# Kernel optimization log

Measured on AMD Instinct MI355X. Metric: run time of the kernel, lower is better.

## Reference

```python
import jax, jax.numpy as jnp
import numpy as np

N = 40000      # nodes
E = 640000     # edges (avg degree 16)
IN = 128       # in_dim
H = 8          # n_heads
D = 16         # out_dim per head
ED = 64        # edge_dim
C = H * D      # out_channel = 128 == IN -> residual is Identity
EPS = 1e-5


def setup_inputs() -> dict:
    key = jax.random.key(0)
    ks = jax.random.split(key, 20)

    def lin(k, shape):
        fan_in = shape[-1]
        return jax.random.normal(k, shape, dtype=jnp.float32) / np.sqrt(fan_in)

    return {
        "q": jax.random.normal(ks[0], (N, IN), dtype=jnp.float32),
        "k": jax.random.normal(ks[1], (N, IN), dtype=jnp.float32),
        "v": jax.random.normal(ks[2], (N, IN), dtype=jnp.float32),
        "edge_feat": jax.random.normal(ks[3], (E, ED), dtype=jnp.float32),
        "src": jax.random.randint(ks[4], (E,), 0, N, dtype=jnp.int32),
        "dst": jax.random.randint(ks[5], (E,), 0, N, dtype=jnp.int32),
        "Wq": lin(ks[6], (C, IN)),
        "Wk": lin(ks[7], (C, IN)),
        "Wv": lin(ks[8], (C, IN)),
        "We": lin(ks[9], (H, ED)),
        "be": jnp.zeros((H,), dtype=jnp.float32),
        "Wo": lin(ks[10], (C, C)),
        "W1": lin(ks[11], (2 * C, C)),
        "b1": jnp.zeros((2 * C,), dtype=jnp.float32),
        "W2": lin(ks[12], (C, 2 * C)),
        "b2": jnp.zeros((C,), dtype=jnp.float32),
        "g1": jnp.ones((C,), dtype=jnp.float32),
        "bt1": jnp.zeros((C,), dtype=jnp.float32),
        "g2": jnp.ones((C,), dtype=jnp.float32),
        "bt2": jnp.zeros((C,), dtype=jnp.float32),
    }


def _batch_norm(x, g, b):
    mu = x.mean(axis=0)
    var = x.var(axis=0)  # biased, matching torch BN normalization
    return (x - mu) * jax.lax.rsqrt(var + EPS) * g + b


def reference(q, k, v, edge_feat, src, dst, Wq, Wk, Wv, We, be, Wo,
              W1, b1, W2, b2, g1, bt1, g2, bt2):
    n = q.shape[0]
    qd = (q @ Wq.T).reshape(n, H, D)        # [N,H,D] dst queries
    ksrc = (k @ Wk.T).reshape(-1, H, D)     # [N,H,D]
    vsrc = (v @ Wv.T).reshape(-1, H, D)     # [N,H,D]

    # per-edge attention scores: v_dot_u(q_dst, k_src) / sqrt(D)
    scores = jnp.einsum('ehd,ehd->eh', qd[dst], ksrc[src]) / jnp.sqrt(jnp.float32(D))
    # edge_mode == 'ADD': add per-head edge bias
    scores = scores + edge_feat @ We.T + be  # [E,H]

    # edge softmax normalized by destination node (segment softmax)
    smax = jax.ops.segment_max(scores, dst, num_segments=n)      # [N,H]
    ex = jnp.exp(scores - smax[dst])
    denom = jax.ops.segment_sum(ex, dst, num_segments=n)         # [N,H]
    attn = ex / denom[dst]                                       # [E,H]

    # scatter-weighted aggregation: sum_e attn * v_src -> dst
    agg = jax.ops.segment_sum(attn[:, :, None] * vsrc[src], dst, num_segments=n)  # [N,H,D]

    rst = agg.reshape(n, C) @ Wo.T
    rst = rst + q                    # residual (Identity: in_dim == out_channel)
    rst = _batch_norm(rst, g1, bt1)

    h = jnp.maximum(rst @ W1.T + b1, 0.0) @ W2.T + b2  # FFN
    rst = _batch_norm(h + rst, g2, bt2)
    return rst
```

## Files before the change

### kernel.cpp

```cpp
#include <hip/hip_runtime.h>
#include <cstdint>
#include <cstddef>

#define Nn 40000
#define Ne 640000
#define CC 128
#define EPSbn 1e-5f

typedef __attribute__((ext_vector_type(8))) __bf16 bf16x8;
typedef __attribute__((ext_vector_type(4))) float floatx4;

__device__ inline unsigned short f2bf(float x){
  union { float f; unsigned u; } c; c.f = x;
  unsigned r = c.u + 0x7fffu + ((c.u >> 16) & 1u);
  return (unsigned short)(r >> 16);
}
__device__ inline float bflo(unsigned u){ return __uint_as_float(u << 16); }
__device__ inline float bfhi(unsigned u){ return __uint_as_float(u & 0xffff0000u); }

__device__ inline unsigned f2e4m3(float x){
  unsigned u = __float_as_uint(x);
  unsigned s = (u >> 24) & 0x80u;
  unsigned a = u & 0x7fffffffu;
  unsigned lsb = (a >> 20) & 1u;
  a += 0x0007FFFFu + lsb;
  int e = (int)((a >> 23) & 0xffu) - 127;
  unsigned b;
  if (e < -9)      b = 0u;
  else if (e < -6) b = (unsigned)(int)rintf(__uint_as_float(u & 0x7fffffffu) * 512.f);
  else if (e > 8)  b = 0x7Eu;
  else             b = (unsigned)(((e + 7) << 3) | ((a >> 20) & 7u));
  if ((b & 0x7fu) == 0x7fu) b = 0x7Eu;
  return s | b;
}

#if defined(__has_builtin)
#if __has_builtin(__builtin_amdgcn_cvt_f32_fp8)
#define FP8_HW 1
#endif
#endif
template<int SEL>
__device__ inline float fp8dec(unsigned w){
#ifdef FP8_HW
  return __builtin_amdgcn_cvt_f32_fp8((int)w, SEL);
#else
  unsigned b = (w >> (SEL*8)) & 0xffu;
  unsigned s = (b & 0x80u) << 24;
  unsigned em = b & 0x7fu;
  float v;
  if (em >= 8) v = __uint_as_float((((em >> 3) + 117u) << 23)) * (float)(8 + (em & 7));
  else         v = (float)em * 0.001953125f;
  return __uint_as_float(__float_as_uint(v) | s);
#endif
}

__global__ void zero_k(int* __restrict__ p, int n){
  int i = blockIdx.x*blockDim.x + threadIdx.x;
  if (i < n) p[i] = 0;
}

struct GA3 {
  const void* A0; const void* A1; const void* A2;
  const float* W0; const float* W1; const float* W2;
  void* C0; void* C1; void* C2;
  int m0, m1, m2;
};

template<int KTILES,bool ABF16,bool HASBIAS,bool HASRES,bool RELU,bool AFFA,bool AFFRES,bool BNSTAT>
__global__ __launch_bounds__(256,2) void mgemm_k(
    GA3 ga, const float* __restrict__ bias, const float* __restrict__ res,
    const float* __restrict__ sc, const float* __restrict__ sh,
    float* __restrict__ bnS, float* __restrict__ bnQ,
    int M, int Ncols)
{
  constexpr int K = KTILES * 128;
  __shared__ __align__(16) unsigned short As[128*136];
  __shared__ __align__(16) unsigned short Ws[128*136];
  const int z = blockIdx.z;
  const void*  Ap = (z==0) ? ga.A0 : (z==1) ? ga.A1 : ga.A2;
  const float* W  = (z==0) ? ga.W0 : (z==1) ? ga.W1 : ga.W2;
  void*        Cp = (z==0) ? ga.C0 : (z==1) ? ga.C1 : ga.C2;
  const int mode  = (z==0) ? ga.m0 : (z==1) ? ga.m1 : ga.m2;

  const int tid  = threadIdx.x;
  const int lane = tid & 63;
  const int wv   = tid >> 6;
  const int m    = lane & 15;
  const int quad = lane >> 4;
  const int row0 = blockIdx.x * 128;
  const int col0 = blockIdx.y * 128;
  floatx4 acc[2][8] = {};

  for (int kt = 0; kt < K; kt += 128) {
    #pragma unroll 4
    for (int it = 0; it < 16; ++it) {
      int s = tid + it*256;
      int r = s >> 5;
      int c = (s & 31) << 2;
      int gr = row0 + r; if (gr >= M) gr = M - 1;
      ushort4 ua;
      if (ABF16) {
        ua = *(const ushort4*)((const unsigned short*)Ap + (size_t)gr*K + kt + c);
      } else {
        float4 a4 = *(const float4*)((const float*)Ap + (size_t)gr*K + kt + c);
        if (AFFA) {
          int kk = kt + c;
          a4.x = a4.x*sc[kk  ] + sh[kk  ];
          a4.y = a4.y*sc[kk+1] + sh[kk+1];
          a4.z = a4.z*sc[kk+2] + sh[kk+2];
          a4.w = a4.w*sc[kk+3] + sh[kk+3];
        }
        ua.x = f2bf(a4.x); ua.y = f2bf(a4.y); ua.z = f2bf(a4.z); ua.w = f2bf(a4.w);
      }
      *(ushort4*)&As[r*136 + c] = ua;
      float4 w4 = *(const float4*)(W + (size_t)(col0 + r)*K + kt + c);
      ushort4 uw;
      uw.x = f2bf(w4.x); uw.y = f2bf(w4.y); uw.z = f2bf(w4.z); uw.w = f2bf(w4.w);
      *(ushort4*)&Ws[r*136 + c] = uw;
    }
    __syncthreads();
    #pragma unroll
    for (int ks = 0; ks < 4; ++ks) {
      int ko = ks*32 + quad*8;
      bf16x8 a0 = *(const bf16x8*)&As[(32*wv      + m)*136 + ko];
      bf16x8 a1 = *(const bf16x8*)&As[(32*wv + 16 + m)*136 + ko];
      #pragma unroll
      for (int j = 0; j < 8; ++j) {
        bf16x8 bj = *(const bf16x8*)&Ws[(16*j + m)*136 + ko];
        acc[0][j] = __builtin_amdgcn_mfma_f32_16x16x32_bf16(a0, bj, acc[0][j], 0, 0, 0);
        acc[1][j] = __builtin_amdgcn_mfma_f32_16x16x32_bf16(a1, bj, acc[1][j], 0, 0, 0);
      }
    }
    __syncthreads();
  }

  float bcol[8], scv[8], shv[8];
  #pragma unroll
  for (int j = 0; j < 8; ++j) {
    int gcol = col0 + 16*j + m;
    if (HASBIAS) bcol[j] = bias[gcol];
    if (AFFRES) { scv[j] = sc[gcol]; shv[j] = sh[gcol]; }
  }
  float ps[8] = {}, pq[8] = {};
  #pragma unroll
  for (int rt = 0; rt < 2; ++rt) {
    #pragma unroll
    for (int rg = 0; rg < 4; ++rg) {
      int grow = row0 + 32*wv + 16*rt + quad*4 + rg;
      if (grow < M) {
        #pragma unroll
        for (int j = 0; j < 8; ++j) {
          int gcol = col0 + 16*j + m;
          float o = acc[rt][j][rg];
          if (HASBIAS) o += bcol[j];
          if (HASRES) {
            float rr = res[(size_t)grow*Ncols + gcol];
            if (AFFRES) rr = rr*scv[j] + shv[j];
            o += rr;
          }
          if (RELU) o = fmaxf(o, 0.f);
          if (BNSTAT) { ps[j] += o; pq[j] += o*o; }
          if (mode == 0) ((float*)Cp)[(size_t)grow*Ncols + gcol] = o;
          else           ((unsigned short*)Cp)[(size_t)grow*Ncols + gcol] = f2bf(o);
        }
      }
    }
  }
  if (BNSTAT) {
    float* sS = (float*)&As[0];
    float* sQ = sS + 4*128;
    #pragma unroll
    for (int j = 0; j < 8; ++j) {
      float s = ps[j], qq = pq[j];
      s += __shfl_xor(s, 16); qq += __shfl_xor(qq, 16);
      s += __shfl_xor(s, 32); qq += __shfl_xor(qq, 32);
      if (quad == 0) { sS[wv*128 + 16*j + m] = s; sQ[wv*128 + 16*j + m] = qq; }
    }
    __syncthreads();
    if (wv == 0) {
      #pragma unroll
      for (int c = 0; c < 128; c += 64) {
        int cc = c + lane;
        float s  = sS[cc] + sS[128+cc] + sS[256+cc] + sS[384+cc];
        float qq = sQ[cc] + sQ[128+cc] + sQ[256+cc] + sQ[384+cc];
        atomicAdd(&bnS[col0 + cc], s);
        atomicAdd(&bnQ[col0 + cc], qq);
      }
    }
  }
}

__global__ __launch_bounds__(256) void repack_k(
    const unsigned* __restrict__ Kb, const unsigned* __restrict__ Vb,
    unsigned* __restrict__ KV, int total)
{
  int i = blockIdx.x*blockDim.x + threadIdx.x;
  if (i < total) {
    unsigned kk = Kb[i];
    unsigned vv = Vb[i];
    unsigned o = f2e4m3(bflo(kk)) | (f2e4m3(bfhi(kk)) << 8)
               | (f2e4m3(bflo(vv)) << 16) | (f2e4m3(bfhi(vv)) << 24);
    KV[i] = o;
  }
}

__global__ __launch_bounds__(256) void ebias_k(
    const float* __restrict__ ef, const float* __restrict__ We,
    const float* __restrict__ be, const int* __restrict__ pos,
    unsigned short* __restrict__ EBs)
{
  __shared__ float efs[32][68];
  __shared__ float Wes[8][68];
  __shared__ float bes[8];
  int tid = threadIdx.x;
  if (tid < 8) bes[tid] = be[tid];
  for (int i = tid; i < 512; i += 256) Wes[i>>6][i&63] = We[i];
  int e0 = blockIdx.x * 32;
  #pragma unroll
  for (int l = 0; l < 2; ++l) {
    int idx = tid + l*256;
    int r   = idx >> 4;
    int q4  = (idx & 15) << 2;
    float4 t = *(const float4*)(ef + (size_t)(e0 + r)*64 + q4);
    efs[r][q4]=t.x; efs[r][q4+1]=t.y; efs[r][q4+2]=t.z; efs[r][q4+3]=t.w;
  }
  __syncthreads();
  int h = tid & 7, el = tid >> 3;
  int e = e0 + el;
  float es = 0.f;
  #pragma unroll
  for (int kk = 0; kk < 64; kk += 4) {
    float4 a = *(const float4*)&efs[el][kk];
    float4 b = *(const float4*)&Wes[h][kk];
    es += a.x*b.x + a.y*b.y + a.z*b.z + a.w*b.w;
  }
  EBs[(size_t)pos[e]*8 + h] = f2bf(es + bes[h]);
}

__global__ void hist_k(const int* __restrict__ dst, int* __restrict__ counts, int E){
  int i = blockIdx.x*blockDim.x + threadIdx.x;
  if (i < E) atomicAdd(&counts[dst[i]], 1);
}

__global__ __launch_bounds__(256) void scan1_k(
    const int* __restrict__ counts, int* __restrict__ part,
    int* __restrict__ bsums, int n)
{
  int tid = threadIdx.x;
  int base = blockIdx.x*1024 + tid*4;
  int v0 = (base   < n) ? counts[base  ] : 0;
  int v1 = (base+1 < n) ? counts[base+1] : 0;
  int v2 = (base+2 < n) ? counts[base+2] : 0;
  int v3 = (base+3 < n) ? counts[base+3] : 0;
  int t1 = v0+v1, t2 = t1+v2, t3 = t2+v3;
  int lane = tid & 63, wv = tid >> 6;
  int x = t3;
  #pragma unroll
  for (int off = 1; off < 64; off <<= 1) {
    int y = __shfl_up(x, off);
    if (lane >= off) x += y;
  }
  __shared__ int wt[4];
  if (lane == 63) wt[wv] = x;
  __syncthreads();
  int wbase = 0;
  #pragma unroll
  for (int w = 0; w < 4; ++w) if (w < wv) wbase += wt[w];
  int excl = wbase + x - t3;
  if (base   < n) part[base  ] = excl;
  if (base+1 < n) part[base+1] = excl + v0;
  if (base+2 < n) part[base+2] = excl + t1;
  if (base+3 < n) part[base+3] = excl + t2;
  if (tid == 255) bsums[blockIdx.x] = wbase + x;
}

__global__ void scan2_k(int* bsums, int nb){
  int lane = threadIdx.x;
  int v = (lane < nb) ? bsums[lane] : 0;
  int x = v;
  #pragma unroll
  for (int off = 1; off < 64; off <<= 1) {
    int y = __shfl_up(x, off);
    if (lane >= off) x += y;
  }
  if (lane < nb) bsums[lane] = x - v;
}

__global__ void scan3_k(int* __restrict__ offsets, const int* __restrict__ bsums,
                        int* __restrict__ cursor, int n, int E){
  int i = blockIdx.x*blockDim.x + threadIdx.x;
  if (i < n) {
    int o = offsets[i] + bsums[i >> 10];
    offsets[i] = o;
    cursor[i]  = o;
  }
  if (i == 0) offsets[n] = E;
}

__global__ void scatter_k(const int* __restrict__ dst, const int* __restrict__ src,
                          int* __restrict__ cursor, int* __restrict__ pos,
                          int* __restrict__ srcs, int E){
  int i = blockIdx.x*blockDim.x + threadIdx.x;
  if (i < E) {
    int p = atomicAdd(&cursor[dst[i]], 1);
    pos[i]  = p;
    srcs[p] = src[i];
  }
}

__global__ __launch_bounds__(256) void agg_k(
    const unsigned* __restrict__ QDb, const unsigned* __restrict__ KV,
    const unsigned short* __restrict__ EBs,
    const int* __restrict__ offsets, const int* __restrict__ srcs,
    float* __restrict__ agg, int n)
{
  int wv = threadIdx.x >> 6, lane = threadIdx.x & 63;
  int node = blockIdx.x*4 + wv;
  if (node >= n) return;
  unsigned qt = QDb[(size_t)node*64 + lane];
  float q0 = bflo(qt) * 0.25f;
  float q1 = bfhi(qt) * 0.25f;
  int beg = offsets[node], end = offsets[node+1];
  int hoff = lane >> 3;
  float acc0 = 0.f, acc1 = 0.f, den = 0.f;
  for (int base = beg; base < end; base += 64) {
    int mrem = end - base; if (mrem > 64) mrem = 64;
    int ss = (lane < mrem) ? srcs[base + lane] : 0;
    int j = 0;
    for (; j + 4 <= mrem; j += 4) {
      int s0 = __shfl(ss, j);
      int s1 = __shfl(ss, j+1);
      int s2 = __shfl(ss, j+2);
      int s3 = __shfl(ss, j+3);
      unsigned kv0 = KV[(size_t)s0*64 + lane];
      unsigned kv1 = KV[(size_t)s1*64 + lane];
      unsigned kv2 = KV[(size_t)s2*64 + lane];
      unsigned kv3 = KV[(size_t)s3*64 + lane];
      float p0 = q0*fp8dec<0>(kv0) + q1*fp8dec<1>(kv0);
      float p1 = q0*fp8dec<0>(kv1) + q1*fp8dec<1>(kv1);
      float p2 = q0*fp8dec<0>(kv2) + q1*fp8dec<1>(kv2);
      float p3 = q0*fp8dec<0>(kv3) + q1*fp8dec<1>(kv3);
      p0 += __shfl_xor(p0, 1); p1 += __shfl_xor(p1, 1); p2 += __shfl_xor(p2, 1); p3 += __shfl_xor(p3, 1);
      p0 += __shfl_xor(p0, 2); p1 += __shfl_xor(p1, 2); p2 += __shfl_xor(p2, 2); p3 += __shfl_xor(p3, 2);
      p0 += __shfl_xor(p0, 4); p1 += __shfl_xor(p1, 4); p2 += __shfl_xor(p2, 4); p3 += __shfl_xor(p3, 4);
      float eb0 = __uint_as_float(((unsigned)EBs[(size_t)(base+j  )*8 + hoff]) << 16);
      float eb1 = __uint_as_float(((unsigned)EBs[(size_t)(base+j+1)*8 + hoff]) << 16);
      float eb2 = __uint_as_float(((unsigned)EBs[(size_t)(base+j+2)*8 + hoff]) << 16);
      float eb3 = __uint_as_float(((unsigned)EBs[(size_t)(base+j+3)*8 + hoff]) << 16);
      float w0 = __expf(p0 + eb0);
      float w1 = __expf(p1 + eb1);
      float w2 = __expf(p2 + eb2);
      float w3 = __expf(p3 + eb3);
      acc0 += w0*fp8dec<2>(kv0) + w1*fp8dec<2>(kv1) + w2*fp8dec<2>(kv2) + w3*fp8dec<2>(kv3);
      acc1 += w0*fp8dec<3>(kv0) + w1*fp8dec<3>(kv1) + w2*fp8dec<3>(kv2) + w3*fp8dec<3>(kv3);
      den  += (w0 + w1) + (w2 + w3);
    }
    for (; j < mrem; ++j) {
      int s0 = __shfl(ss, j);
      unsigned kv0 = KV[(size_t)s0*64 + lane];
      float p0 = q0*fp8dec<0>(kv0) + q1*fp8dec<1>(kv0);
      p0 += __shfl_xor(p0, 1);
      p0 += __shfl_xor(p0, 2);
      p0 += __shfl_xor(p0, 4);
      float eb0 = __uint_as_float(((unsigned)EBs[(size_t)(base+j)*8 + hoff]) << 16);
      float w0 = __expf(p0 + eb0);
      acc0 += w0*fp8dec<2>(kv0);
      acc1 += w0*fp8dec<3>(kv0);
      den  += w0;
    }
  }
  float inv = den > 0.f ? 1.f/den : 0.f;
  float2 o; o.x = acc0*inv; o.y = acc1*inv;
  *(float2*)(agg + (size_t)node*128 + 2*lane) = o;
}

__global__ void bnfin_k(const float* sum, const float* sq, const float* g,
                        const float* bt, float* scale, float* shift, int M){
  int c = threadIdx.x;
  float mu  = sum[c] / (float)M;
  float var = sq[c] / (float)M - mu*mu;
  float s = g[c] * rsqrtf(var + EPSbn);
  scale[c] = s;
  shift[c] = bt[c] - mu*s;
}

__global__ void bnapply_k(const float* __restrict__ Y, const float* __restrict__ scale,
                          const float* __restrict__ shift, float* __restrict__ out, int total){
  int n4 = total >> 2;
  for (int i = blockIdx.x*blockDim.x + threadIdx.x; i < n4; i += gridDim.x*blockDim.x) {
    float4 vv = ((const float4*)Y)[i];
    int c = (i << 2) & 127;
    vv.x = vv.x*scale[c  ] + shift[c  ];
    vv.y = vv.y*scale[c+1] + shift[c+1];
    vv.z = vv.z*scale[c+2] + shift[c+2];
    vv.w = vv.w*scale[c+3] + shift[c+3];
    ((float4*)out)[i] = vv;
  }
}

extern "C" void kernel_launch(void* const* d_in, const int* in_sizes, int n_in,
                              void* d_out, int out_size, void* d_ws, size_t ws_size,
                              hipStream_t stream) {
  const float* q   = (const float*)d_in[0];
  const float* k   = (const float*)d_in[1];
  const float* v   = (const float*)d_in[2];
  const float* ef  = (const float*)d_in[3];
  const int*   src = (const int*)d_in[4];
  const int*   dst = (const int*)d_in[5];
  const float* Wq  = (const float*)d_in[6];
  const float* Wk  = (const float*)d_in[7];
  const float* Wv  = (const float*)d_in[8];
  const float* We  = (const float*)d_in[9];
  const float* be  = (const float*)d_in[10];
  const float* Wo  = (const float*)d_in[11];
  const float* W1  = (const float*)d_in[12];
  const float* b1  = (const float*)d_in[13];
  const float* W2  = (const float*)d_in[14];
  const float* b2  = (const float*)d_in[15];
  const float* g1  = (const float*)d_in[16];
  const float* bt1 = (const float*)d_in[17];
  const float* g2  = (const float*)d_in[18];
  const float* bt2 = (const float*)d_in[19];
  float* out = (float*)d_out;

  float* ws = (float*)d_ws;
  const size_t NB = (size_t)Nn * CC;
  float* QDb = ws;
  float* Kb  = ws + NB/2;
  float* Vb  = ws + NB;
  unsigned* KVq = (unsigned*)(ws + 3*NB/2);
  unsigned short* EBs = (unsigned short*)(ws + 2*NB);
  float* AGG = ws + 5*NB/2;
  float* RST = ws + 7*NB/2;
  float* H1  = ws;
  float* Y   = AGG;
  float* bn = ws + 9*NB/2;
  float* sum1 = bn;       float* sq1 = bn+128;  float* sc1 = bn+256; float* sh1 = bn+384;
  float* sum2 = bn+512;   float* sq2 = bn+640;  float* sc2 = bn+768; float* sh2 = bn+896;
  int* ib      = (int*)(bn + 1024);
  int* counts  = ib;
  int* offsets = ib + 40000;
  int* cursor  = ib + 80001;
  int* posA    = ib + 120001;
  int* srcsA   = ib + 760001;
  int* bsums   = ib + 1400001;

  zero_k<<<dim3(161), 256, 0, stream>>>((int*)bn, 1024 + Nn);

  hist_k<<<dim3(2500), 256, 0, stream>>>(dst, counts, Ne);
  scan1_k<<<dim3(40), 256, 0, stream>>>(counts, offsets, bsums, Nn);
  scan2_k<<<dim3(1), 64, 0, stream>>>(bsums, 40);
  scan3_k<<<dim3(157), 256, 0, stream>>>(offsets, bsums, cursor, Nn, Ne);
  scatter_k<<<dim3(2500), 256, 0, stream>>>(dst, src, cursor, posA, srcsA, Ne);

  {
    GA3 ga;
    ga.A0 = q;  ga.A1 = k;  ga.A2 = v;
    ga.W0 = Wq; ga.W1 = Wk; ga.W2 = Wv;
    ga.C0 = QDb; ga.C1 = Kb; ga.C2 = Vb;
    ga.m0 = 1; ga.m1 = 1; ga.m2 = 1;
    mgemm_k<1,false,false,false,false,false,false,false><<<dim3(313,1,3),256,0,stream>>>(
        ga, nullptr, nullptr, nullptr, nullptr, nullptr, nullptr, Nn, 128);
  }

  repack_k<<<dim3(10000), 256, 0, stream>>>((const unsigned*)Kb, (const unsigned*)Vb,
                                            KVq, Nn*64);

  ebias_k<<<dim3(Ne/32), 256, 0, stream>>>(ef, We, be, posA, EBs);

  agg_k<<<dim3(Nn/4), 256, 0, stream>>>((const unsigned*)QDb, KVq, EBs,
                                        offsets, srcsA, AGG, Nn);

  {
    GA3 ga = {};
    ga.A0 = AGG; ga.W0 = Wo; ga.C0 = RST; ga.m0 = 0;
    mgemm_k<1,false,false,true,false,false,false,true><<<dim3(313,1,1),256,0,stream>>>(
        ga, nullptr, q, nullptr, nullptr, sum1, sq1, Nn, 128);
  }
  bnfin_k<<<dim3(1), 128, 0, stream>>>(sum1, sq1, g1, bt1, sc1, sh1, Nn);

  {
    GA3 ga = {};
    ga.A0 = RST; ga.W0 = W1; ga.C0 = H1; ga.m0 = 1;
    mgemm_k<1,false,true,false,true,true,false,false><<<dim3(313,2,1),256,0,stream>>>(
        ga, b1, nullptr, sc1, sh1, nullptr, nullptr, Nn, 256);
  }

  {
    GA3 ga = {};
    ga.A0 = H1; ga.W0 = W2; ga.C0 = Y; ga.m0 = 0;
    mgemm_k<2,true,true,true,false,false,true,true><<<dim3(313,1,1),256,0,stream>>>(
        ga, b2, RST, sc1, sh1, sum2, sq2, Nn, 128);
  }
  bnfin_k<<<dim3(1), 128, 0, stream>>>(sum2, sq2, g2, bt2, sc2, sh2, Nn);
  bnapply_k<<<dim3(1024), 256, 0, stream>>>(Y, sc2, sh2, out, Nn*CC);
}
```

Measured before the change: 543.4 us.

## Pre-convert weights to bf16, fuse repack and BN finalize into neighboring kernels

Weights are converted to bf16 once in a prep kernel that also zeroes the workspace, so the GEMM tile loads become plain 16-byte copies instead of fp32 loads plus conversion. The K/V projection GEMM now writes fp8 directly into the interleaved KV layout, which removes the repack kernel and its intermediate bf16 buffers. Aggregation output is stored as bf16, halving the Wo GEMM input traffic. The BN finalize kernels are folded into the consuming GEMMs and the final apply kernel, cutting launches at the cost of every block recomputing the 128-channel scale and shift, and the fp8 output path does scattered byte stores.

```diff
diff --git a/kernel.cpp b/kernel.cpp
--- a/kernel.cpp
+++ b/kernel.cpp
@@ -9,6 +9,7 @@
 
 typedef __attribute__((ext_vector_type(8))) __bf16 bf16x8;
 typedef __attribute__((ext_vector_type(4))) float floatx4;
+typedef __attribute__((ext_vector_type(8))) unsigned short ushort8;
 
 __device__ inline unsigned short f2bf(float x){
   union { float f; unsigned u; } c; c.f = x;
@@ -54,33 +55,49 @@
 #endif
 }
 
-__global__ void zero_k(int* __restrict__ p, int n){
-  int i = blockIdx.x*blockDim.x + threadIdx.x;
-  if (i < n) p[i] = 0;
+__global__ __launch_bounds__(256) void prep_k(int* __restrict__ zp, int zn,
+    const float* __restrict__ Wq, const float* __restrict__ Wk,
+    const float* __restrict__ Wv, const float* __restrict__ Wo,
+    const float* __restrict__ W1, const float* __restrict__ W2,
+    unsigned short* __restrict__ Wb)
+{
+  int b = blockIdx.x, tid = threadIdx.x;
+  if (b < 161) { int i = b*256 + tid; if (i < zn) zp[i] = 0; return; }
+  int i = (b - 161)*256 + tid;
+  const float* s; int off;
+  if      (i < 16384) { s = Wq; off = i; }
+  else if (i < 32768) { s = Wk; off = i - 16384; }
+  else if (i < 49152) { s = Wv; off = i - 32768; }
+  else if (i < 65536) { s = Wo; off = i - 49152; }
+  else if (i < 98304) { s = W1; off = i - 65536; }
+  else                { s = W2; off = i - 98304; }
+  Wb[i] = f2bf(s[off]);
 }
 
 struct GA3 {
   const void* A0; const void* A1; const void* A2;
-  const float* W0; const float* W1; const float* W2;
+  const unsigned short* W0; const unsigned short* W1; const unsigned short* W2;
   void* C0; void* C1; void* C2;
   int m0, m1, m2;
 };
 
-template<int KTILES,bool ABF16,bool HASBIAS,bool HASRES,bool RELU,bool AFFA,bool AFFRES,bool BNSTAT>
+template<int KTILES,bool ABF16,bool HASBIAS,bool HASRES,bool RELU,bool BNA,bool BNRES,bool BNSTAT>
 __global__ __launch_bounds__(256,2) void mgemm_k(
     GA3 ga, const float* __restrict__ bias, const float* __restrict__ res,
-    const float* __restrict__ sc, const float* __restrict__ sh,
+    const float* __restrict__ bnSin, const float* __restrict__ bnQin,
+    const float* __restrict__ gamma, const float* __restrict__ beta,
     float* __restrict__ bnS, float* __restrict__ bnQ,
     int M, int Ncols)
 {
   constexpr int K = KTILES * 128;
   __shared__ __align__(16) unsigned short As[128*136];
   __shared__ __align__(16) unsigned short Ws[128*136];
+  __shared__ float scb[128], shb[128];
   const int z = blockIdx.z;
-  const void*  Ap = (z==0) ? ga.A0 : (z==1) ? ga.A1 : ga.A2;
-  const float* W  = (z==0) ? ga.W0 : (z==1) ? ga.W1 : ga.W2;
-  void*        Cp = (z==0) ? ga.C0 : (z==1) ? ga.C1 : ga.C2;
-  const int mode  = (z==0) ? ga.m0 : (z==1) ? ga.m1 : ga.m2;
+  const void*           Ap = (z==0) ? ga.A0 : (z==1) ? ga.A1 : ga.A2;
+  const unsigned short* W  = (z==0) ? ga.W0 : (z==1) ? ga.W1 : ga.W2;
+  void*                 Cp = (z==0) ? ga.C0 : (z==1) ? ga.C1 : ga.C2;
+  const int mode           = (z==0) ? ga.m0 : (z==1) ? ga.m1 : ga.m2;
 
   const int tid  = threadIdx.x;
   const int lane = tid & 63;
@@ -89,34 +106,57 @@
   const int quad = lane >> 4;
   const int row0 = blockIdx.x * 128;
   const int col0 = blockIdx.y * 128;
+
+  if (BNA || BNRES) {
+    if (tid < 128) {
+      float mu  = bnSin[tid] / (float)M;
+      float var = bnQin[tid] / (float)M - mu*mu;
+      float s   = gamma[tid] * rsqrtf(var + EPSbn);
+      scb[tid] = s;
+      shb[tid] = beta[tid] - mu*s;
+    }
+    __syncthreads();
+  }
+
   floatx4 acc[2][8] = {};
 
   for (int kt = 0; kt < K; kt += 128) {
-    #pragma unroll 4
-    for (int it = 0; it < 16; ++it) {
+    #pragma unroll
+    for (int it = 0; it < 8; ++it) {
       int s = tid + it*256;
-      int r = s >> 5;
-      int c = (s & 31) << 2;
-      int gr = row0 + r; if (gr >= M) gr = M - 1;
-      ushort4 ua;
-      if (ABF16) {
-        ua = *(const ushort4*)((const unsigned short*)Ap + (size_t)gr*K + kt + c);
-      } else {
+      int r = s >> 4;
+      int c = (s & 15) << 3;
+      *(ushort8*)&Ws[r*136 + c] =
+          *(const ushort8*)(W + (size_t)(col0 + r)*K + kt + c);
+    }
+    if (ABF16) {
+      #pragma unroll
+      for (int it = 0; it < 8; ++it) {
+        int s = tid + it*256;
+        int r = s >> 4;
+        int c = (s & 15) << 3;
+        int gr = row0 + r; if (gr >= M) gr = M - 1;
+        *(ushort8*)&As[r*136 + c] =
+            *(const ushort8*)((const unsigned short*)Ap + (size_t)gr*K + kt + c);
+      }
+    } else {
+      #pragma unroll 4
+      for (int it = 0; it < 16; ++it) {
+        int s = tid + it*256;
+        int r = s >> 5;
+        int c = (s & 31) << 2;
+        int gr = row0 + r; if (gr >= M) gr = M - 1;
         float4 a4 = *(const float4*)((const float*)Ap + (size_t)gr*K + kt + c);
-        if (AFFA) {
-          int kk = kt + c;
-          a4.x = a4.x*sc[kk  ] + sh[kk  ];
-          a4.y = a4.y*sc[kk+1] + sh[kk+1];
-          a4.z = a4.z*sc[kk+2] + sh[kk+2];
-          a4.w = a4.w*sc[kk+3] + sh[kk+3];
+        if (BNA) {
+          a4.x = a4.x*scb[c  ] + shb[c  ];
+          a4.y = a4.y*scb[c+1] + shb[c+1];
+          a4.z = a4.z*scb[c+2] + shb[c+2];
+          a4.w = a4.w*scb[c+3] + shb[c+3];
         }
+        ushort4 ua;
         ua.x = f2bf(a4.x); ua.y = f2bf(a4.y); ua.z = f2bf(a4.z); ua.w = f2bf(a4.w);
+        *(ushort4*)&As[r*136 + c] = ua;
       }
-      *(ushort4*)&As[r*136 + c] = ua;
-      float4 w4 = *(const float4*)(W + (size_t)(col0 + r)*K + kt + c);
-      ushort4 uw;
-      uw.x = f2bf(w4.x); uw.y = f2bf(w4.y); uw.z = f2bf(w4.z); uw.w = f2bf(w4.w);
-      *(ushort4*)&Ws[r*136 + c] = uw;
     }
     __syncthreads();
     #pragma unroll
@@ -139,7 +179,7 @@
   for (int j = 0; j < 8; ++j) {
     int gcol = col0 + 16*j + m;
     if (HASBIAS) bcol[j] = bias[gcol];
-    if (AFFRES) { scv[j] = sc[gcol]; shv[j] = sh[gcol]; }
+    if (BNRES) { scv[j] = scb[16*j + m]; shv[j] = shb[16*j + m]; }
   }
   float ps[8] = {}, pq[8] = {};
   #pragma unroll
@@ -155,13 +195,19 @@
           if (HASBIAS) o += bcol[j];
           if (HASRES) {
             float rr = res[(size_t)grow*Ncols + gcol];
-            if (AFFRES) rr = rr*scv[j] + shv[j];
+            if (BNRES) rr = rr*scv[j] + shv[j];
             o += rr;
           }
           if (RELU) o = fmaxf(o, 0.f);
           if (BNSTAT) { ps[j] += o; pq[j] += o*o; }
-          if (mode == 0) ((float*)Cp)[(size_t)grow*Ncols + gcol] = o;
-          else           ((unsigned short*)Cp)[(size_t)grow*Ncols + gcol] = f2bf(o);
+          if (mode == 0)      ((float*)Cp)[(size_t)grow*Ncols + gcol] = o;
+          else if (mode == 1) ((unsigned short*)Cp)[(size_t)grow*Ncols + gcol] = f2bf(o);
+          else {
+            float obf = __uint_as_float(((unsigned)f2bf(o)) << 16);
+            size_t boff = (size_t)grow*256 + (size_t)((gcol >> 1) << 2)
+                        + (gcol & 1) + ((mode == 3) ? 2 : 0);
+            ((unsigned char*)Cp)[boff] = (unsigned char)f2e4m3(obf);
+          }
         }
       }
     }
@@ -187,20 +233,6 @@
         atomicAdd(&bnQ[col0 + cc], qq);
       }
     }
-  }
-}
-
-__global__ __launch_bounds__(256) void repack_k(
-    const unsigned* __restrict__ Kb, const unsigned* __restrict__ Vb,
-    unsigned* __restrict__ KV, int total)
-{
-  int i = blockIdx.x*blockDim.x + threadIdx.x;
-  if (i < total) {
-    unsigned kk = Kb[i];
-    unsigned vv = Vb[i];
-    unsigned o = f2e4m3(bflo(kk)) | (f2e4m3(bfhi(kk)) << 8)
-               | (f2e4m3(bflo(vv)) << 16) | (f2e4m3(bfhi(vv)) << 24);
-    KV[i] = o;
   }
 }
 
@@ -312,7 +344,7 @@
     const unsigned* __restrict__ QDb, const unsigned* __restrict__ KV,
     const unsigned short* __restrict__ EBs,
     const int* __restrict__ offsets, const int* __restrict__ srcs,
-    float* __restrict__ agg, int n)
+    unsigned* __restrict__ agg, int n)
 {
   int wv = threadIdx.x >> 6, lane = threadIdx.x & 63;
   int node = blockIdx.x*4 + wv;
@@ -370,30 +402,34 @@
     }
   }
   float inv = den > 0.f ? 1.f/den : 0.f;
-  float2 o; o.x = acc0*inv; o.y = acc1*inv;
-  *(float2*)(agg + (size_t)node*128 + 2*lane) = o;
-}
-
-__global__ void bnfin_k(const float* sum, const float* sq, const float* g,
-                        const float* bt, float* scale, float* shift, int M){
-  int c = threadIdx.x;
-  float mu  = sum[c] / (float)M;
-  float var = sq[c] / (float)M - mu*mu;
-  float s = g[c] * rsqrtf(var + EPSbn);
-  scale[c] = s;
-  shift[c] = bt[c] - mu*s;
-}
-
-__global__ void bnapply_k(const float* __restrict__ Y, const float* __restrict__ scale,
-                          const float* __restrict__ shift, float* __restrict__ out, int total){
+  unsigned o = (unsigned)f2bf(acc0*inv) | ((unsigned)f2bf(acc1*inv) << 16);
+  agg[(size_t)node*64 + lane] = o;
+}
+
+__global__ __launch_bounds__(256) void bnapply_k(
+    const float* __restrict__ Y,
+    const float* __restrict__ sum2, const float* __restrict__ sq2,
+    const float* __restrict__ g, const float* __restrict__ bt,
+    float* __restrict__ out, int M, int total)
+{
+  __shared__ float scb[128], shb[128];
+  int tid = threadIdx.x;
+  if (tid < 128) {
+    float mu  = sum2[tid] / (float)M;
+    float var = sq2[tid] / (float)M - mu*mu;
+    float s   = g[tid] * rsqrtf(var + EPSbn);
+    scb[tid] = s;
+    shb[tid] = bt[tid] - mu*s;
+  }
+  __syncthreads();
   int n4 = total >> 2;
-  for (int i = blockIdx.x*blockDim.x + threadIdx.x; i < n4; i += gridDim.x*blockDim.x) {
+  for (int i = blockIdx.x*blockDim.x + tid; i < n4; i += gridDim.x*blockDim.x) {
     float4 vv = ((const float4*)Y)[i];
     int c = (i << 2) & 127;
-    vv.x = vv.x*scale[c  ] + shift[c  ];
-    vv.y = vv.y*scale[c+1] + shift[c+1];
-    vv.z = vv.z*scale[c+2] + shift[c+2];
-    vv.w = vv.w*scale[c+3] + shift[c+3];
+    vv.x = vv.x*scb[c  ] + shb[c  ];
+    vv.y = vv.y*scb[c+1] + shb[c+1];
+    vv.z = vv.z*scb[c+2] + shb[c+2];
+    vv.w = vv.w*scb[c+3] + shb[c+3];
     ((float4*)out)[i] = vv;
   }
 }
@@ -426,17 +462,15 @@
   float* ws = (float*)d_ws;
   const size_t NB = (size_t)Nn * CC;
   float* QDb = ws;
-  float* Kb  = ws + NB/2;
-  float* Vb  = ws + NB;
   unsigned* KVq = (unsigned*)(ws + 3*NB/2);
   unsigned short* EBs = (unsigned short*)(ws + 2*NB);
-  float* AGG = ws + 5*NB/2;
+  unsigned* AGGb = (unsigned*)(ws + 5*NB/2);
+  float* Y   = ws + 5*NB/2;
   float* RST = ws + 7*NB/2;
   float* H1  = ws;
-  float* Y   = AGG;
   float* bn = ws + 9*NB/2;
-  float* sum1 = bn;       float* sq1 = bn+128;  float* sc1 = bn+256; float* sh1 = bn+384;
-  float* sum2 = bn+512;   float* sq2 = bn+640;  float* sc2 = bn+768; float* sh2 = bn+896;
+  float* sum1 = bn;       float* sq1 = bn+128;
+  float* sum2 = bn+512;   float* sq2 = bn+640;
   int* ib      = (int*)(bn + 1024);
   int* counts  = ib;
   int* offsets = ib + 40000;
@@ -444,8 +478,16 @@
   int* posA    = ib + 120001;
   int* srcsA   = ib + 760001;
   int* bsums   = ib + 1400001;
-
-  zero_k<<<dim3(161), 256, 0, stream>>>((int*)bn, 1024 + Nn);
+  unsigned short* Wb = (unsigned short*)(ib + 1400068);
+  unsigned short* WqB = Wb;
+  unsigned short* WkB = Wb + 16384;
+  unsigned short* WvB = Wb + 32768;
+  unsigned short* WoB = Wb + 49152;
+  unsigned short* W1B = Wb + 65536;
+  unsigned short* W2B = Wb + 98304;
+
+  prep_k<<<dim3(673), 256, 0, stream>>>((int*)bn, 1024 + Nn,
+                                        Wq, Wk, Wv, Wo, W1, W2, Wb);
 
   hist_k<<<dim3(2500), 256, 0, stream>>>(dst, counts, Ne);
   scan1_k<<<dim3(40), 256, 0, stream>>>(counts, offsets, bsums, Nn);
@@ -455,43 +497,43 @@
 
   {
     GA3 ga;
-    ga.A0 = q;  ga.A1 = k;  ga.A2 = v;
-    ga.W0 = Wq; ga.W1 = Wk; ga.W2 = Wv;
-    ga.C0 = QDb; ga.C1 = Kb; ga.C2 = Vb;
-    ga.m0 = 1; ga.m1 = 1; ga.m2 = 1;
+    ga.A0 = q;   ga.A1 = k;   ga.A2 = v;
+    ga.W0 = WqB; ga.W1 = WkB; ga.W2 = WvB;
+    ga.C0 = QDb; ga.C1 = KVq; ga.C2 = KVq;
+    ga.m0 = 1;   ga.m1 = 2;   ga.m2 = 3;
     mgemm_k<1,false,false,false,false,false,false,false><<<dim3(313,1,3),256,0,stream>>>(
-        ga, nullptr, nullptr, nullptr, nullptr, nullptr, nullptr, Nn, 128);
-  }
-
-  repack_k<<<dim3(10000), 256, 0, stream>>>((const unsigned*)Kb, (const unsigned*)Vb,
-                                            KVq, Nn*64);
+        ga, nullptr, nullptr, nullptr, nullptr, nullptr, nullptr,
+        nullptr, nullptr, Nn, 128);
+  }
 
   ebias_k<<<dim3(Ne/32), 256, 0, stream>>>(ef, We, be, posA, EBs);
 
   agg_k<<<dim3(Nn/4), 256, 0, stream>>>((const unsigned*)QDb, KVq, EBs,
-                                        offsets, srcsA, AGG, Nn);
+                                        offsets, srcsA, AGGb, Nn);
 
   {
     GA3 ga = {};
-    ga.A0 = AGG; ga.W0 = Wo; ga.C0 = RST; ga.m0 = 0;
-    mgemm_k<1,false,false,true,false,false,false,true><<<dim3(313,1,1),256,0,stream>>>(
-        ga, nullptr, q, nullptr, nullptr, sum1, sq1, Nn, 128);
-  }
-  bnfin_k<<<dim3(1), 128, 0, stream>>>(sum1, sq1, g1, bt1, sc1, sh1, Nn);
+    ga.A0 = AGGb; ga.W0 = WoB; ga.C0 = RST; ga.m0 = 0;
+    mgemm_k<1,true,false,true,false,false,false,true><<<dim3(313,1,1),256,0,stream>>>(
+        ga, nullptr, q, nullptr, nullptr, nullptr, nullptr,
+        sum1, sq1, Nn, 128);
+  }
 
   {
     GA3 ga = {};
-    ga.A0 = RST; ga.W0 = W1; ga.C0 = H1; ga.m0 = 1;
+    ga.A0 = RST; ga.W0 = W1B; ga.C0 = H1; ga.m0 = 1;
     mgemm_k<1,false,true,false,true,true,false,false><<<dim3(313,2,1),256,0,stream>>>(
-        ga, b1, nullptr, sc1, sh1, nullptr, nullptr, Nn, 256);
+        ga, b1, nullptr, sum1, sq1, g1, bt1,
+        nullptr, nullptr, Nn, 256);
   }
 
   {
     GA3 ga = {};
-    ga.A0 = H1; ga.W0 = W2; ga.C0 = Y; ga.m0 = 0;
+    ga.A0 = H1; ga.W0 = W2B; ga.C0 = Y; ga.m0 = 0;
     mgemm_k<2,true,true,true,false,false,true,true><<<dim3(313,1,1),256,0,stream>>>(
-        ga, b2, RST, sc1, sh1, sum2, sq2, Nn, 128);
-  }
-  bnfin_k<<<dim3(1), 128, 0, stream>>>(sum2, sq2, g2, bt2, sc2, sh2, Nn);
-  bnapply_k<<<dim3(1024), 256, 0, stream>>>(Y, sc2, sh2, out, Nn*CC);
-}
+        ga, b2, RST, sum1, sq1, g1, bt1,
+        sum2, sq2, Nn, 128);
+  }
+
+  bnapply_k<<<dim3(1024), 256, 0, stream>>>(Y, sum2, sq2, g2, bt2, out, Nn, Nn*CC);
+}
```

Measured after the change: 558.2 us. +2.7%, slower.
